# Kernel optimization log

Hardware: AMD Instinct MI355X
Metric: run time of the kernel (lower is better)

Reference implementation:

```python
import jax, jax.numpy as jnp
import numpy as np

B, S, D_MODEL, D_INNER = 64, 128, 1024, 1024


def setup_inputs() -> dict:
    key = jax.random.key(0)
    ks = jax.random.split(key, 10)
    sc = 0.02
    return {
        "embeddings": jax.random.normal(ks[0], (B, S, D_MODEL), dtype=jnp.float32),
        "Wq": jax.random.normal(ks[1], (D_MODEL, D_INNER), dtype=jnp.float32) * sc,
        "bq": jnp.zeros((D_INNER,), dtype=jnp.float32),
        "Wk": jax.random.normal(ks[2], (D_MODEL, D_INNER), dtype=jnp.float32) * sc,
        "bk": jnp.zeros((D_INNER,), dtype=jnp.float32),
        "Wv": jax.random.normal(ks[3], (D_MODEL, D_INNER), dtype=jnp.float32) * sc,
        "bv": jnp.zeros((D_INNER,), dtype=jnp.float32),
        "w": jax.random.normal(ks[4], (S, S), dtype=jnp.float32) * sc,
        "Wo": jax.random.normal(ks[5], (D_INNER, D_MODEL), dtype=jnp.float32) * sc,
        "bo": jnp.zeros((D_MODEL,), dtype=jnp.float32),
    }


def reference(embeddings, Wq, bq, Wk, bk, Wv, bv, w, Wo, bo):
    # embeddings: [B, S, Dm]
    seq_len = embeddings.shape[1]
    q = embeddings @ Wq + bq          # [B, S, Di]
    k = embeddings @ Wk + bk
    v = embeddings @ Wv + bv

    max_k = jnp.max(k, axis=1, keepdims=True)   # [B, 1, Di]
    exp_k = jnp.exp(k - max_k)                  # [B, S, Di]

    max_w = jnp.max(w, axis=1, keepdims=True)   # [S, 1]
    wn = w - max_w                              # [S, S]
    tril = jnp.tril(jnp.ones((seq_len, seq_len), dtype=bool))
    wn = jnp.where(tril, wn[:seq_len, :seq_len], -jnp.inf)
    # torch.einsum('bjj,bjd->bjd', exp_w, x) picks the DIAGONAL of exp_w
    # (repeated subscript j) and multiplies elementwise along the seq dim.
    diag_w = jnp.exp(jnp.diagonal(wn))          # [S]; tril diagonal is True so finite
    dw = diag_w[None, :, None]                  # [1, S, 1]

    numerator = dw * (exp_k * v)                # [B, S, Di]
    denominator = dw * exp_k                    # [B, S, Di]
    out = jax.nn.sigmoid(q) * (numerator / denominator)
    return out @ Wo + bo                        # [B, S, Dm]
```

## Files before the change

kernel.cpp:

```cpp
#include <hip/hip_runtime.h>


typedef short bf16x8 __attribute__((ext_vector_type(8)));
typedef float f32x4  __attribute__((ext_vector_type(4)));

__device__ __forceinline__ short f2bf(float f) {
  union { float f; unsigned u; } x; x.f = f;
  unsigned r = x.u + 0x7fffu + ((x.u >> 16) & 1u);
  return (short)(r >> 16);
}

struct alignas(16) S8 { short v[8]; };

#define GLDS(g, l) \
  __builtin_amdgcn_global_load_lds((const __attribute__((address_space(1))) void*)(g), \
                                   (__attribute__((address_space(3))) void*)(l), 16, 0, 0)
#define BAR()    __builtin_amdgcn_s_barrier()
#define PRIO(x)  __builtin_amdgcn_s_setprio(x)
#define SCHED0() __builtin_amdgcn_sched_barrier(0)
#define VMCNT(N) asm volatile("s_waitcnt vmcnt(" #N ")" ::: "memory")
#define LGKM0()  asm volatile("s_waitcnt lgkmcnt(0)" ::: "memory")
#define MFMA(a, b, c) __builtin_amdgcn_mfma_f32_16x16x32_bf16((a), (b), (c), 0, 0, 0)

__global__ __launch_bounds__(256) void prep_kernel(
    const float* __restrict__ emb, const float* __restrict__ Wq, const float* __restrict__ Wv,
    const float* __restrict__ Wo, short* __restrict__ embB, short* __restrict__ WqvT,
    short* __restrict__ WoT) {
  __shared__ float tr[64 * 65];
  const int t = threadIdx.x;
  const int bid = blockIdx.x;
  const int gdim = gridDim.x;

  for (size_t i = (size_t)bid * 256 + t; i < 1048576; i += (size_t)gdim * 256) {
    const float4* p = (const float4*)emb + i * 2;
    float4 a = p[0], b = p[1];
    S8 s;
    s.v[0] = f2bf(a.x); s.v[1] = f2bf(a.y); s.v[2] = f2bf(a.z); s.v[3] = f2bf(a.w);
    s.v[4] = f2bf(b.x); s.v[5] = f2bf(b.y); s.v[6] = f2bf(b.z); s.v[7] = f2bf(b.w);
    ((S8*)embB)[i] = s;
  }

  const int rr = t >> 4, cc4 = (t & 15) * 4;
  const int orow = t >> 3, ocol8 = (t & 7) * 8;
  for (int z = bid; z < 768; z += gdim) {
    const float* in; short* op; int ti;
    if (z < 256)      { in = Wq; op = WqvT;           ti = z; }
    else if (z < 512) { in = Wv; op = WqvT + 1048576; ti = z - 256; }
    else              { in = Wo; op = WoT;            ti = z - 512; }
    const int bx = (ti & 15) * 64, by = (ti >> 4) * 64;
    __syncthreads();
#pragma unroll
    for (int k = 0; k < 4; ++k) {
      float4 v = *(const float4*)&in[(size_t)(by + rr + 16 * k) * 1024 + bx + cc4];
      float* d = &tr[(rr + 16 * k) * 65 + cc4];
      d[0] = v.x; d[1] = v.y; d[2] = v.z; d[3] = v.w;
    }
    __syncthreads();
#pragma unroll
    for (int h = 0; h < 2; ++h) {
      const int oc = orow + 32 * h;
      S8 s;
#pragma unroll
      for (int i = 0; i < 8; ++i) s.v[i] = f2bf(tr[(ocol8 + i) * 65 + oc]);
      *(S8*)&op[(size_t)(bx + oc) * 1024 + by + ocol8] = s;
    }
  }
}

__global__ __launch_bounds__(512, 2) void gemm_qv_kernel(
    const short* __restrict__ A, const short* __restrict__ BT,
    const float* __restrict__ bq, const float* __restrict__ bv, short* __restrict__ X) {
  __shared__ short As[2][256 * 64];
  __shared__ short Bqs[2][128 * 64];
  __shared__ short Bvs[2][128 * 64];
  const int t = threadIdx.x;
  const int lane = t & 63;
  const int w = t >> 6;
  const int l16 = lane & 15;
  const int quad = lane >> 4;
  const int b = blockIdx.x;
  const int wg = (b & 7) * 32 + (b >> 3);
  const int bm = (wg >> 3) * 256;
  const int bn = (wg & 7) * 128;
  const int wm = (w & 3) * 64;
  const int wn = (w >> 2) * 64;

  const int r8 = t >> 3;
  const int swe = ((t & 7) ^ (r8 & 7)) * 8;
  const short* gA = A + (size_t)(bm + r8) * 1024 + swe;
  const short* gq = BT + (size_t)(bn + r8) * 1024 + swe;
  const short* gv = BT + (size_t)(1024 + bn + r8) * 1024 + swe;
  short* lA = &As[0][0] + w * 512;
  short* lq = &Bqs[0][0] + w * 512;
  short* lv = &Bvs[0][0] + w * 512;

#define QV_STAGE(k, s) do {                                             \
    const short* a_ = gA + (k) * 64; short* la_ = lA + (s) * 16384;     \
    GLDS(a_, la_);               GLDS(a_ + 64 * 1024, la_ + 4096);      \
    GLDS(a_ + 128 * 1024, la_ + 8192); GLDS(a_ + 192 * 1024, la_ + 12288); \
    const short* q_ = gq + (k) * 64; short* lq_ = lq + (s) * 8192;      \
    GLDS(q_, lq_);               GLDS(q_ + 64 * 1024, lq_ + 4096);      \
    const short* v_ = gv + (k) * 64; short* lv_ = lv + (s) * 8192;      \
    GLDS(v_, lv_);               GLDS(v_ + 64 * 1024, lv_ + 4096);      \
  } while (0)

  const int csw0 = (quad ^ (l16 & 7)) * 8;
  const int csw1 = ((quad + 4) ^ (l16 & 7)) * 8;
  const short* fA0 = &As[0][0] + (wm + l16) * 64 + csw0;
  const short* fA1 = &As[0][0] + (wm + l16) * 64 + csw1;
  const short* fq0 = &Bqs[0][0] + (wn + l16) * 64 + csw0;
  const short* fq1 = &Bqs[0][0] + (wn + l16) * 64 + csw1;
  const short* fv0 = &Bvs[0][0] + (wn + l16) * 64 + csw0;
  const short* fv1 = &Bvs[0][0] + (wn + l16) * 64 + csw1;

  f32x4 aq[4][4] = {};
  f32x4 av[4][4] = {};

  QV_STAGE(0, 0);
  QV_STAGE(1, 1);

  for (int j = 0; j < 16; ++j) {
    const int s = j & 1;
    const short* sA0 = fA0 + s * 16384;
    const short* sA1 = fA1 + s * 16384;
    const short* sq0 = fq0 + s * 8192;
    const short* sq1 = fq1 + s * 8192;
    const short* sv0 = fv0 + s * 8192;
    const short* sv1 = fv1 + s * 8192;

    if (j < 15) { VMCNT(8); } else { VMCNT(0); }
    BAR();

    bf16x8 a0[4], a1[4], bq0[4], bq1[4], bv0[4], bv1[4];
#pragma unroll
    for (int i = 0; i < 4; ++i) {
      a0[i] = *(const bf16x8*)(sA0 + i * 1024);
      a1[i] = *(const bf16x8*)(sA1 + i * 1024);
      bq0[i] = *(const bf16x8*)(sq0 + i * 1024);
    }
    BAR(); LGKM0(); SCHED0(); PRIO(1);
#pragma unroll
    for (int i = 0; i < 4; ++i)
#pragma unroll
      for (int n = 0; n < 4; ++n)
        aq[i][n] = MFMA(a0[i], bq0[n], aq[i][n]);
    PRIO(0); BAR();
#pragma unroll
    for (int i = 0; i < 4; ++i) {
      bq1[i] = *(const bf16x8*)(sq1 + i * 1024);
      bv0[i] = *(const bf16x8*)(sv0 + i * 1024);
      bv1[i] = *(const bf16x8*)(sv1 + i * 1024);
    }
    BAR(); LGKM0(); SCHED0(); PRIO(1);
#pragma unroll
    for (int i = 0; i < 4; ++i)
#pragma unroll
      for (int n = 0; n < 4; ++n)
        aq[i][n] = MFMA(a1[i], bq1[n], aq[i][n]);
    PRIO(0); BAR();
    if (j < 14) {
      const short* a_ = gA + (j + 2) * 64; short* la_ = lA + s * 16384;
      GLDS(a_, la_);                     GLDS(a_ + 64 * 1024, la_ + 4096);
      GLDS(a_ + 128 * 1024, la_ + 8192); GLDS(a_ + 192 * 1024, la_ + 12288);
    }
    PRIO(1);
#pragma unroll
    for (int i = 0; i < 4; ++i)
#pragma unroll
      for (int n = 0; n < 4; ++n)
        av[i][n] = MFMA(a0[i], bv0[n], av[i][n]);
    PRIO(0); BAR();
    if (j < 14) {
      const short* q_ = gq + (j + 2) * 64; short* lq_ = lq + s * 8192;
      GLDS(q_, lq_); GLDS(q_ + 64 * 1024, lq_ + 4096);
      const short* v_ = gv + (j + 2) * 64; short* lv_ = lv + s * 8192;
      GLDS(v_, lv_); GLDS(v_ + 64 * 1024, lv_ + 4096);
    }
    PRIO(1);
#pragma unroll
    for (int i = 0; i < 4; ++i)
#pragma unroll
      for (int n = 0; n < 4; ++n)
        av[i][n] = MFMA(a1[i], bv1[n], av[i][n]);
    PRIO(0); BAR();
  }
#undef QV_STAGE

#pragma unroll
  for (int n = 0; n < 4; ++n) {
    const int col = bn + wn + n * 16 + l16;
    const float bql = bq[col], bvl = bv[col];
#pragma unroll
    for (int i = 0; i < 4; ++i)
#pragma unroll
      for (int r = 0; r < 4; ++r) {
        const int row = bm + wm + i * 16 + quad * 4 + r;
        const float q = aq[i][n][r] + bql;
        const float v = av[i][n][r] + bvl;
        const float sg = 1.0f / (1.0f + __expf(-q));
        X[(size_t)row * 1024 + col] = f2bf(sg * v);
      }
  }
}

__global__ __launch_bounds__(256) void gemm_bt_kernel(
    const short* __restrict__ A, const short* __restrict__ BT, float* __restrict__ C,
    const float* __restrict__ bias) {
  __shared__ short As[128 * 64];
  __shared__ short Bs[128 * 64];
  const int t = threadIdx.x;
  const int lane = t & 63;
  const int w = t >> 6;
  const int l16 = lane & 15;
  const int quad = lane >> 4;
  const int bm = blockIdx.x * 128;
  const int bn = blockIdx.y * 128;
  const int wm = (w & 1) * 64;
  const int wn = (w >> 1) * 64;

  const int r8 = t >> 3;
  const int swe = ((t & 7) ^ (r8 & 7)) * 8;
  const short* pA0 = A + (size_t)(bm + r8) * 1024 + swe;
  const short* pA1 = pA0 + 32 * 1024;
  const short* pA2 = pA0 + 64 * 1024;
  const short* pA3 = pA0 + 96 * 1024;
  const short* pB0 = BT + (size_t)(bn + r8) * 1024 + swe;
  const short* pB1 = pB0 + 32 * 1024;
  const short* pB2 = pB0 + 64 * 1024;
  const short* pB3 = pB0 + 96 * 1024;
  short* lA = As + w * 512;
  short* lB = Bs + w * 512;

  const int qsw0 = (quad ^ (l16 & 7)) * 8;
  const int qsw1 = ((quad + 4) ^ (l16 & 7)) * 8;
  const short* fA0 = As + (wm + l16) * 64 + qsw0;
  const short* fA1 = As + (wm + l16) * 64 + qsw1;
  const short* fB0 = Bs + (wn + l16) * 64 + qsw0;
  const short* fB1 = Bs + (wn + l16) * 64 + qsw1;

  f32x4 acc[4][4] = {};

  for (int it = 0; it < 16; ++it) {
    GLDS(pA0, lA); GLDS(pA1, lA + 2048); GLDS(pA2, lA + 4096); GLDS(pA3, lA + 6144);
    GLDS(pB0, lB); GLDS(pB1, lB + 2048); GLDS(pB2, lB + 4096); GLDS(pB3, lB + 6144);
    pA0 += 64; pA1 += 64; pA2 += 64; pA3 += 64;
    pB0 += 64; pB1 += 64; pB2 += 64; pB3 += 64;
    __syncthreads();

#pragma unroll
    for (int h = 0; h < 2; h++) {
      const short* fA = h ? fA1 : fA0;
      const short* fB = h ? fB1 : fB0;
      bf16x8 av[4], bw[4];
#pragma unroll
      for (int i = 0; i < 4; i++) av[i] = *(const bf16x8*)(fA + i * 1024);
#pragma unroll
      for (int j = 0; j < 4; j++) bw[j] = *(const bf16x8*)(fB + j * 1024);
#pragma unroll
      for (int i = 0; i < 4; i++)
#pragma unroll
        for (int j = 0; j < 4; j++)
          acc[i][j] = MFMA(av[i], bw[j], acc[i][j]);
    }
    __syncthreads();
  }

#pragma unroll
  for (int j = 0; j < 4; j++) {
    int col = bn + wn + j * 16 + l16;
    float bl = bias[col];
#pragma unroll
    for (int i = 0; i < 4; i++)
#pragma unroll
      for (int r = 0; r < 4; r++) {
        int row = bm + wm + i * 16 + quad * 4 + r;
        C[(size_t)row * 1024 + col] = acc[i][j][r] + bl;
      }
  }
}

extern "C" void kernel_launch(void* const* d_in, const int* in_sizes, int n_in,
                              void* d_out, int out_size, void* d_ws, size_t ws_size,
                              hipStream_t stream) {
  const float* emb = (const float*)d_in[0];
  const float* Wq  = (const float*)d_in[1];
  const float* bq  = (const float*)d_in[2];
  const float* Wv  = (const float*)d_in[5];
  const float* bv  = (const float*)d_in[6];
  const float* Wo  = (const float*)d_in[8];
  const float* bo  = (const float*)d_in[9];
  float* out = (float*)d_out;

  char* ws = (char*)d_ws;
  short* embB = (short*)(ws);
  short* X    = (short*)(ws + 16777216);
  short* WqvT = (short*)(ws + 33554432);
  short* WoT  = (short*)(ws + 37748736);

  prep_kernel<<<768, 256, 0, stream>>>(emb, Wq, Wv, Wo, embB, WqvT, WoT);
  gemm_qv_kernel<<<256, 512, 0, stream>>>(embB, WqvT, bq, bv, X);
  gemm_bt_kernel<<<dim3(64, 8), 256, 0, stream>>>(X, WoT, out, bo);
}
```

Baseline: 162.8 us.

## Simplify QV GEMM main loop: fewer barriers, interleave Q/V MFMAs per k-half

Restructures the fused Q/V projection inner loop. It drops the four intermediate barriers and scheduling fences, loads the A, Q and V fragments together for each k-half, and interleaves the Q and V MFMAs. A single barrier then issues the next stage's global-to-LDS prefetch. This cuts barrier and synchronization overhead and lets the compiler schedule LDS reads with MFMAs. In exchange, the prefetch issues later in the iteration, which shrinks overlap with compute, and the compiler's own scheduling may be worse than the hand-tuned order.

```diff
diff --git a/kernel.cpp b/kernel.cpp
--- a/kernel.cpp
+++ b/kernel.cpp
@@ -17,7 +17,6 @@
                                    (__attribute__((address_space(3))) void*)(l), 16, 0, 0)
 #define BAR()    __builtin_amdgcn_s_barrier()
 #define PRIO(x)  __builtin_amdgcn_s_setprio(x)
-#define SCHED0() __builtin_amdgcn_sched_barrier(0)
 #define VMCNT(N) asm volatile("s_waitcnt vmcnt(" #N ")" ::: "memory")
 #define LGKM0()  asm volatile("s_waitcnt lgkmcnt(0)" ::: "memory")
 #define MFMA(a, b, c) __builtin_amdgcn_mfma_f32_16x16x32_bf16((a), (b), (c), 0, 0, 0)
@@ -131,58 +130,46 @@
     if (j < 15) { VMCNT(8); } else { VMCNT(0); }
     BAR();
 
-    bf16x8 a0[4], a1[4], bq0[4], bq1[4], bv0[4], bv1[4];
-#pragma unroll
-    for (int i = 0; i < 4; ++i) {
-      a0[i] = *(const bf16x8*)(sA0 + i * 1024);
-      a1[i] = *(const bf16x8*)(sA1 + i * 1024);
-      bq0[i] = *(const bf16x8*)(sq0 + i * 1024);
-    }
-    BAR(); LGKM0(); SCHED0(); PRIO(1);
-#pragma unroll
-    for (int i = 0; i < 4; ++i)
-#pragma unroll
-      for (int n = 0; n < 4; ++n)
-        aq[i][n] = MFMA(a0[i], bq0[n], aq[i][n]);
-    PRIO(0); BAR();
-#pragma unroll
-    for (int i = 0; i < 4; ++i) {
-      bq1[i] = *(const bf16x8*)(sq1 + i * 1024);
-      bv0[i] = *(const bf16x8*)(sv0 + i * 1024);
-      bv1[i] = *(const bf16x8*)(sv1 + i * 1024);
-    }
-    BAR(); LGKM0(); SCHED0(); PRIO(1);
-#pragma unroll
-    for (int i = 0; i < 4; ++i)
-#pragma unroll
-      for (int n = 0; n < 4; ++n)
-        aq[i][n] = MFMA(a1[i], bq1[n], aq[i][n]);
-    PRIO(0); BAR();
-    if (j < 14) {
-      const short* a_ = gA + (j + 2) * 64; short* la_ = lA + s * 16384;
-      GLDS(a_, la_);                     GLDS(a_ + 64 * 1024, la_ + 4096);
-      GLDS(a_ + 128 * 1024, la_ + 8192); GLDS(a_ + 192 * 1024, la_ + 12288);
-    }
-    PRIO(1);
-#pragma unroll
-    for (int i = 0; i < 4; ++i)
-#pragma unroll
-      for (int n = 0; n < 4; ++n)
-        av[i][n] = MFMA(a0[i], bv0[n], av[i][n]);
-    PRIO(0); BAR();
-    if (j < 14) {
-      const short* q_ = gq + (j + 2) * 64; short* lq_ = lq + s * 8192;
-      GLDS(q_, lq_); GLDS(q_ + 64 * 1024, lq_ + 4096);
-      const short* v_ = gv + (j + 2) * 64; short* lv_ = lv + s * 8192;
-      GLDS(v_, lv_); GLDS(v_ + 64 * 1024, lv_ + 4096);
-    }
-    PRIO(1);
-#pragma unroll
-    for (int i = 0; i < 4; ++i)
-#pragma unroll
-      for (int n = 0; n < 4; ++n)
-        av[i][n] = MFMA(a1[i], bv1[n], av[i][n]);
-    PRIO(0); BAR();
+    {
+      bf16x8 a0[4], bq0[4], bv0[4];
+#pragma unroll
+      for (int i = 0; i < 4; ++i) {
+        a0[i] = *(const bf16x8*)(sA0 + i * 1024);
+        bq0[i] = *(const bf16x8*)(sq0 + i * 1024);
+        bv0[i] = *(const bf16x8*)(sv0 + i * 1024);
+      }
+      PRIO(1);
+#pragma unroll
+      for (int i = 0; i < 4; ++i)
+#pragma unroll
+        for (int n = 0; n < 4; ++n) {
+          aq[i][n] = MFMA(a0[i], bq0[n], aq[i][n]);
+          av[i][n] = MFMA(a0[i], bv0[n], av[i][n]);
+        }
+      PRIO(0);
+    }
+    {
+      bf16x8 a1[4], bq1[4], bv1[4];
+#pragma unroll
+      for (int i = 0; i < 4; ++i) {
+        a1[i] = *(const bf16x8*)(sA1 + i * 1024);
+        bq1[i] = *(const bf16x8*)(sq1 + i * 1024);
+        bv1[i] = *(const bf16x8*)(sv1 + i * 1024);
+      }
+      PRIO(1);
+#pragma unroll
+      for (int i = 0; i < 4; ++i)
+#pragma unroll
+        for (int n = 0; n < 4; ++n) {
+          aq[i][n] = MFMA(a1[i], bq1[n], aq[i][n]);
+          av[i][n] = MFMA(a1[i], bv1[n], av[i][n]);
+        }
+      PRIO(0);
+    }
+
+    LGKM0();
+    BAR();
+    if (j < 14) QV_STAGE(j + 2, s);
   }
 #undef QV_STAGE
 
```

New measurement: 164.1 us. No clear change (+0.8%).
